# Optimization experiments

Hardware: AMD Instinct MI355X
Metric: run time of the kernel (lower is better)

## Reference

```python
import jax, jax.numpy as jnp
import numpy as np

DIM = 1024
N_HEADS = 16
HEAD_DIM = DIM // N_HEADS


def setup_inputs() -> dict:
    key = jax.random.key(0)
    kx, kq, kk, kv, ko = jax.random.split(key, 5)
    B, S = 2, 2048
    scale = 1.0 / np.sqrt(DIM)
    return {
        "x": jax.random.normal(kx, (B, S, DIM), dtype=jnp.float32),
        "Wq": jax.random.normal(kq, (DIM, DIM), dtype=jnp.float32) * scale,
        "Wk": jax.random.normal(kk, (DIM, DIM), dtype=jnp.float32) * scale,
        "Wv": jax.random.normal(kv, (DIM, DIM), dtype=jnp.float32) * scale,
        "Wo": jax.random.normal(ko, (DIM, DIM), dtype=jnp.float32) * scale,
    }


def rotate_half(x):
    x1, x2 = jnp.split(x, 2, axis=-1)
    return jnp.concatenate([-x2, x1], axis=-1)


def rope_freqs(seq_len, dim):
    inv_freq = 1.0 / (10000.0 ** (jnp.arange(0, dim, 2, dtype=jnp.float32) / dim))
    t = jnp.arange(seq_len, dtype=jnp.float32)
    freqs = jnp.einsum('i,j->ij', t, inv_freq)  # [S, dim/2]
    return jnp.concatenate([freqs, freqs], axis=-1)  # [S, dim]


def apply_rotary(x, freqs):
    # x: [B, H, S, Dh], freqs: [S, Dh]
    cos = jnp.cos(freqs)[None, None]
    sin = jnp.sin(freqs)[None, None]
    return x * cos + rotate_half(x) * sin


def reference(x, Wq, Wk, Wv, Wo):
    B, S, D = x.shape
    H, Dh = N_HEADS, HEAD_DIM
    # nn.Linear(dim, dim, bias=False): y = x @ W.T
    q = (x @ Wq.T).reshape(B, S, H, Dh).transpose(0, 2, 1, 3)
    k = (x @ Wk.T).reshape(B, S, H, Dh).transpose(0, 2, 1, 3)
    v = (x @ Wv.T).reshape(B, S, H, Dh).transpose(0, 2, 1, 3)
    freqs = rope_freqs(S, Dh)
    q = apply_rotary(q, freqs)
    k = apply_rotary(k, freqs)
    attn = jnp.einsum('bhqd,bhkd->bhqk', q, k) / jnp.sqrt(jnp.float32(Dh))
    attn = jax.nn.softmax(attn, axis=-1)
    out = jnp.einsum('bhqk,bhkd->bhqd', attn, v)
    out = out.transpose(0, 2, 1, 3).reshape(B, S, D)
    return out @ Wo.T
```

## Files before the change

kernel.cpp:

```cpp
#include <hip/hip_runtime.h>
#include <hip/hip_bf16.h>

#define NB 2
#define NS 2048
#define ND 1024
#define NH 16
#define NDH 64
#define NM 4096
#define KVT 4096
#define KVBH (NS * NDH)

typedef __bf16 bf16;
typedef __bf16 bf16x8 __attribute__((ext_vector_type(8)));
typedef __bf16 bf16x4 __attribute__((ext_vector_type(4)));
typedef float f32x4 __attribute__((ext_vector_type(4)));
typedef float f32x16 __attribute__((ext_vector_type(16)));

#define ASYNC16(g, l) __builtin_amdgcn_global_load_lds( \
    (const __attribute__((address_space(1))) void*)(g), \
    (__attribute__((address_space(3))) void*)(l), 16, 0, 0)

static __device__ __forceinline__ unsigned cvt_pk_bf16(float a, float b) {
  unsigned r;
  asm("v_cvt_pk_bf16_f32 %0, %1, %2" : "=v"(r) : "v"(a), "v"(b));
  return r;
}

__global__ __launch_bounds__(256) void convert_kernel(
    const float* __restrict__ x,
    const float* __restrict__ wq, const float* __restrict__ wk,
    const float* __restrict__ wv, const float* __restrict__ wo,
    bf16* __restrict__ xb, bf16* __restrict__ wb) {
  int i = blockIdx.x * 256 + threadIdx.x;
  const int n_x4 = (NM * ND) / 4;
  const int n_w4 = (ND * ND) / 4;
  float4 v;
  bf16* dst;
  if (i < n_x4) {
    v = ((const float4*)x)[i];
    dst = xb + (size_t)i * 4;
  } else {
    int j = i - n_x4;
    int w = j / n_w4;
    int o = j - w * n_w4;
    const float* W = (w == 0) ? wq : (w == 1) ? wk : (w == 2) ? wv : wo;
    v = ((const float4*)W)[o];
    dst = wb + (size_t)w * (ND * ND) + (size_t)o * 4;
  }
  bf16x4 o4;
  o4[0] = (bf16)v.x; o4[1] = (bf16)v.y; o4[2] = (bf16)v.z; o4[3] = (bf16)v.w;
  *(bf16x4*)dst = o4;
}

__global__ __launch_bounds__(256) void tab_kernel(float2* __restrict__ tab) {
  int t = blockIdx.x * 256 + threadIdx.x;
  int s = t >> 5, d = t & 31;
  float invf = exp2f(-0.4152410118609203f * (float)d);
  float f = (float)s * invf;
  float sn, cs;
  sincosf(f, &sn, &cs);
  tab[t] = make_float2(cs, sn);
}

__global__ __launch_bounds__(256) void gemm_qkv(
    const bf16* __restrict__ A, const bf16* __restrict__ Bmat,
    bf16* __restrict__ Qr, bf16* __restrict__ Kg, bf16* __restrict__ vraw,
    const float2* __restrict__ tab) {
  __shared__ bf16 As[128 * 64];
  __shared__ bf16 Bs[128 * 64];
  const int t = threadIdx.x;
  const int lane = t & 63, w = t >> 6;
  const int wr = w >> 1, wc = w & 1;
  const int bm = blockIdx.y * 128;
  const int bn = blockIdx.x * 128;
  const int z = blockIdx.z;
  const bf16* Bz = Bmat + (size_t)z * ND * ND;

  f32x4 acc[4][4];
#pragma unroll
  for (int i = 0; i < 4; ++i)
#pragma unroll
    for (int j = 0; j < 4; ++j) acc[i][j] = (f32x4){0.f, 0.f, 0.f, 0.f};

  for (int kt = 0; kt < ND / 64; ++kt) {
    __syncthreads();
#pragma unroll
    for (int i = 0; i < 4; ++i) {
      int c = w * 64 + lane + i * 256;
      int row = c >> 3;
      int js = (c & 7) ^ (row & 7);
      ASYNC16(A + (size_t)(bm + row) * ND + kt * 64 + js * 8, As + c * 8);
      ASYNC16(Bz + (size_t)(bn + row) * ND + kt * 64 + js * 8, Bs + c * 8);
    }
    __syncthreads();
#pragma unroll
    for (int ks = 0; ks < 2; ++ks) {
      const int kb = ks * 64 + (lane >> 4) * 16;
      bf16x8 af[4], bfr[4];
#pragma unroll
      for (int i = 0; i < 4; ++i) {
        int ra = wr * 64 + i * 16 + (lane & 15);
        af[i] = *(const bf16x8*)((const char*)As + ra * 128 + (kb ^ ((ra & 7) << 4)));
        int rb = wc * 64 + i * 16 + (lane & 15);
        bfr[i] = *(const bf16x8*)((const char*)Bs + rb * 128 + (kb ^ ((rb & 7) << 4)));
      }
#pragma unroll
      for (int i = 0; i < 4; ++i)
#pragma unroll
        for (int j = 0; j < 4; ++j)
          acc[i][j] = __builtin_amdgcn_mfma_f32_16x16x32_bf16(af[i], bfr[j], acc[i][j], 0, 0, 0);
    }
  }

  const int row0 = bm + wr * 64;
  const int col0 = bn + wc * 64;
  if (z == 2) {
#pragma unroll
    for (int i = 0; i < 4; ++i)
#pragma unroll
      for (int j = 0; j < 4; ++j) {
        int r = row0 + i * 16 + (lane >> 4) * 4;
        int ccol = col0 + j * 16 + (lane & 15);
#pragma unroll
        for (int q = 0; q < 4; ++q)
          vraw[(size_t)(r + q) * ND + ccol] = (bf16)acc[i][j][q];
      }
  } else {
    const float qs = z ? 1.0f : 0.1803368801111204f;
    const int h = col0 >> 6;
    const int ln15 = lane & 15;
#pragma unroll
    for (int i = 0; i < 4; ++i)
#pragma unroll
      for (int j = 0; j < 2; ++j)
#pragma unroll
        for (int q = 0; q < 4; ++q) {
          int r = row0 + i * 16 + (lane >> 4) * 4 + q;
          int b = r >> 11, s = r & (NS - 1);
          int d1 = j * 16 + ln15;
          float2 tc = tab[s * 32 + d1];
          float x1 = acc[i][j][q], x2 = acc[i][j + 2][q];
          float y1 = (x1 * tc.x - x2 * tc.y) * qs;
          float y2 = (x2 * tc.x + x1 * tc.y) * qs;
          if (z == 0) {
            size_t base = ((size_t)((b * NH + h) * NS + s)) * NDH;
            Qr[base + d1]      = (bf16)y1;
            Qr[base + d1 + 32] = (bf16)y2;
          } else {
            size_t kb2 = ((size_t)(b * NH + h)) * KVBH + (size_t)(s >> 6) * KVT + (s & 63) * 8;
            int cp1 = d1 >> 3, e1 = d1 & 7;
            Kg[kb2 + cp1 * 512 + e1]       = (bf16)y1;
            Kg[kb2 + (cp1 + 4) * 512 + e1] = (bf16)y2;
          }
        }
  }
}

__global__ __launch_bounds__(256) void gemm_out(
    const bf16* __restrict__ A, const bf16* __restrict__ Bmat,
    float* __restrict__ Cout) {
  __shared__ bf16 As[128 * 64];
  __shared__ bf16 Bs[64 * 64];
  const int t = threadIdx.x;
  const int lane = t & 63, w = t >> 6;
  const int wr = w >> 1, wc = w & 1;
  const int bm = blockIdx.y * 128;
  const int bn = blockIdx.x * 64;

  f32x4 acc[4][2];
#pragma unroll
  for (int i = 0; i < 4; ++i)
#pragma unroll
    for (int j = 0; j < 2; ++j) acc[i][j] = (f32x4){0.f, 0.f, 0.f, 0.f};

  for (int kt = 0; kt < ND / 64; ++kt) {
    __syncthreads();
#pragma unroll
    for (int i = 0; i < 4; ++i) {
      int c = i * 256 + t;
      int row = c >> 3;
      int js = (c & 7) ^ (row & 7);
      ASYNC16(A + (size_t)(bm + row) * ND + kt * 64 + js * 8, As + c * 8);
    }
#pragma unroll
    for (int i = 0; i < 2; ++i) {
      int c = i * 256 + t;
      int row = c >> 3;
      int js = (c & 7) ^ (row & 7);
      ASYNC16(Bmat + (size_t)(bn + row) * ND + kt * 64 + js * 8, Bs + c * 8);
    }
    __syncthreads();
#pragma unroll
    for (int ks = 0; ks < 2; ++ks) {
      const int kb = ks * 64 + (lane >> 4) * 16;
      bf16x8 af[4], bfr[2];
#pragma unroll
      for (int i = 0; i < 4; ++i) {
        int ra = wr * 64 + i * 16 + (lane & 15);
        af[i] = *(const bf16x8*)((const char*)As + ra * 128 + (kb ^ ((ra & 7) << 4)));
      }
#pragma unroll
      for (int j = 0; j < 2; ++j) {
        int rb = wc * 32 + j * 16 + (lane & 15);
        bfr[j] = *(const bf16x8*)((const char*)Bs + rb * 128 + (kb ^ ((rb & 7) << 4)));
      }
#pragma unroll
      for (int i = 0; i < 4; ++i)
#pragma unroll
        for (int j = 0; j < 2; ++j)
          acc[i][j] = __builtin_amdgcn_mfma_f32_16x16x32_bf16(af[i], bfr[j], acc[i][j], 0, 0, 0);
    }
  }

  const int row0 = bm + wr * 64;
  const int col0 = bn + wc * 32;
#pragma unroll
  for (int i = 0; i < 4; ++i)
#pragma unroll
    for (int j = 0; j < 2; ++j) {
      int r = row0 + i * 16 + (lane >> 4) * 4;
      int ccol = col0 + j * 16 + (lane & 15);
#pragma unroll
      for (int q = 0; q < 4; ++q)
        Cout[(size_t)(r + q) * ND + ccol] = acc[i][j][q];
    }
}

__global__ __launch_bounds__(256) void transv_kernel(
    const bf16* __restrict__ vraw, bf16* __restrict__ Vg) {
  __shared__ bf16 tl[64][65];
  int s0 = blockIdx.x * 64;
  int bh = blockIdx.y;
  int b = bh >> 4, h = bh & 15;
  int t = threadIdx.x;
#pragma unroll
  for (int i = 0; i < 4; ++i) {
    int row = (t >> 4) + i * 16;
    int d4 = (t & 15) * 4;
    *(bf16x4*)&tl[row][d4] =
        *(const bf16x4*)&vraw[((size_t)(b * NS + s0 + row)) * ND + h * NDH + d4];
  }
  __syncthreads();
  const size_t tbase = (size_t)bh * KVBH + (size_t)(s0 >> 6) * KVT;
#pragma unroll
  for (int i = 0; i < 4; ++i) {
    int dr = (t >> 4) + i * 16;
    int s4 = (t & 15) * 4;
    bf16x4 o;
    o[0] = tl[s4 + 0][dr]; o[1] = tl[s4 + 1][dr];
    o[2] = tl[s4 + 2][dr]; o[3] = tl[s4 + 3][dr];
    *(bf16x4*)&Vg[tbase + (s4 >> 3) * 512 + dr * 8 + (s4 & 7)] = o;
  }
}

__global__ __launch_bounds__(256, 2) void attn_kernel(
    const bf16* __restrict__ Qr, const bf16* __restrict__ Kg,
    const bf16* __restrict__ Vg, bf16* __restrict__ out) {
  __shared__ bf16 Ks[2][512 * 8];
  __shared__ bf16 Vs[2][512 * 8];
  const int t = threadIdx.x, lane = t & 63, w = t >> 6;
  const int hi = lane >> 5, ln = lane & 31;
  int wg = blockIdx.x;
  int sw = (wg & 7) * 64 + (wg >> 3);
  const int qb = sw & 15, bh = sw >> 4;
  const int q0 = qb * 128 + w * 32;
  const size_t kvbase = (size_t)bh * KVBH;

  bf16x8 qv[4];
  {
    const bf16* Qb = Qr + ((size_t)bh * NS + q0 + ln) * NDH + hi * 8;
#pragma unroll
    for (int c = 0; c < 4; ++c) qv[c] = *(const bf16x8*)(Qb + c * 16);
  }

  f32x16 O0, O1;
#pragma unroll
  for (int r = 0; r < 16; ++r) { O0[r] = 0.f; O1[r] = 0.f; }
  float m = -1e30f, l = 0.f;

#define STAGE_KV(nb, kt2)                                                     \
  {                                                                           \
    _Pragma("unroll")                                                         \
    for (int i = 0; i < 2; ++i) {                                             \
      int ch = i * 256 + t;                                                   \
      ASYNC16(Kg + kvbase + (size_t)(kt2) * KVT + ch * 8, &Ks[nb][0] + ch * 8); \
      ASYNC16(Vg + kvbase + (size_t)(kt2) * KVT + ch * 8, &Vs[nb][0] + ch * 8); \
    }                                                                         \
  }

  STAGE_KV(0, 0);
  __syncthreads();

  int cur = 0;
  for (int kt = 0; kt < NS / 64; ++kt) {
    if (kt + 1 < NS / 64) STAGE_KV(cur ^ 1, kt + 1);
    const bf16* Kb = &Ks[cur][0];
    const bf16* Vb = &Vs[cur][0];

    f32x16 s0, s1;
#pragma unroll
    for (int r = 0; r < 16; ++r) { s0[r] = 0.f; s1[r] = 0.f; }
    bf16x8 k0[4], k1[4];
#pragma unroll
    for (int c = 0; c < 4; ++c) {
      k0[c] = *(const bf16x8*)(Kb + (2 * c + hi) * 512 + ln * 8);
      k1[c] = *(const bf16x8*)(Kb + (2 * c + hi) * 512 + (32 + ln) * 8);
    }
    __builtin_amdgcn_s_setprio(1);
#pragma unroll
    for (int c = 0; c < 4; ++c) {
      s0 = __builtin_amdgcn_mfma_f32_32x32x16_bf16(k0[c], qv[c], s0, 0, 0, 0);
      s1 = __builtin_amdgcn_mfma_f32_32x32x16_bf16(k1[c], qv[c], s1, 0, 0, 0);
    }
    __builtin_amdgcn_s_setprio(0);

    float a0[8];
#pragma unroll
    for (int r = 0; r < 8; ++r) a0[r] = fmaxf(fmaxf(s0[r], s0[r + 8]), fmaxf(s1[r], s1[r + 8]));
    float b0 = fmaxf(fmaxf(a0[0], a0[1]), fmaxf(a0[2], a0[3]));
    float b1 = fmaxf(fmaxf(a0[4], a0[5]), fmaxf(a0[6], a0[7]));
    float pmax = fmaxf(b0, b1);
    pmax = fmaxf(pmax, __shfl_xor(pmax, 32, 64));

    if (!__all(pmax - m <= 8.0f)) {
      float mnew = fmaxf(m, pmax);
      float scl = exp2f(m - mnew);
      m = mnew; l *= scl;
#pragma unroll
      for (int r = 0; r < 16; ++r) { O0[r] *= scl; O1[r] *= scl; }
    }

    float p0[16], p1[16];
#pragma unroll
    for (int r = 0; r < 16; ++r) { p0[r] = exp2f(s0[r] - m); p1[r] = exp2f(s1[r] - m); }
    float sp[8];
#pragma unroll
    for (int r = 0; r < 8; ++r) sp[r] = (p0[r] + p0[r + 8]) + (p1[r] + p1[r + 8]);
    float sum = (((sp[0] + sp[1]) + (sp[2] + sp[3])) + ((sp[4] + sp[5]) + (sp[6] + sp[7])));
    sum += __shfl_xor(sum, 32, 64);
    l += sum;

    unsigned u0[8], u1[8], x0[8], x1[8];
#pragma unroll
    for (int g = 0; g < 4; ++g) {
      u0[g]     = cvt_pk_bf16(p0[4 * g],     p0[4 * g + 1]);
      u1[g]     = cvt_pk_bf16(p0[4 * g + 2], p0[4 * g + 3]);
      u0[4 + g] = cvt_pk_bf16(p1[4 * g],     p1[4 * g + 1]);
      u1[4 + g] = cvt_pk_bf16(p1[4 * g + 2], p1[4 * g + 3]);
    }
#pragma unroll
    for (int g = 0; g < 8; ++g) {
      x0[g] = __shfl_xor(u0[g], 32, 64);
      x1[g] = __shfl_xor(u1[g], 32, 64);
    }

    bf16x8 v0[4], v1[4];
#pragma unroll
    for (int c = 0; c < 4; ++c) {
      v0[c] = *(const bf16x8*)(Vb + (2 * c + hi) * 512 + ln * 8);
      v1[c] = *(const bf16x8*)(Vb + (2 * c + hi) * 512 + (32 + ln) * 8);
    }
    __builtin_amdgcn_s_setprio(1);
#pragma unroll
    for (int c = 0; c < 4; ++c) {
      int base = (c >> 1) * 4 + (c & 1) * 2;
      union { unsigned u[4]; bf16x8 v; } pa;
      pa.u[0] = hi ? x0[base + 1] : u0[base];
      pa.u[1] = hi ? x1[base + 1] : u1[base];
      pa.u[2] = hi ? u0[base + 1] : x0[base];
      pa.u[3] = hi ? u1[base + 1] : x1[base];
      O0 = __builtin_amdgcn_mfma_f32_32x32x16_bf16(pa.v, v0[c], O0, 0, 0, 0);
      O1 = __builtin_amdgcn_mfma_f32_32x32x16_bf16(pa.v, v1[c], O1, 0, 0, 0);
    }
    __builtin_amdgcn_s_setprio(0);

    __syncthreads();
    cur ^= 1;
  }

  float rl = 1.0f / l;
  const int b = bh >> 4, h = bh & 15;
#pragma unroll
  for (int r = 0; r < 16; ++r) {
    int q = (r & 3) + 8 * (r >> 2) + 4 * hi;
    float rlq = __shfl(rl, q, 64);
    int s = q0 + q;
    size_t base = ((size_t)(b * NS + s)) * ND + h * NDH + ln;
    out[base]      = (bf16)(O0[r] * rlq);
    out[base + 32] = (bf16)(O1[r] * rlq);
  }
}

extern "C" void kernel_launch(void* const* d_in, const int* in_sizes, int n_in,
                              void* d_out, int out_size, void* d_ws, size_t ws_size,
                              hipStream_t stream) {
  const float* x  = (const float*)d_in[0];
  const float* wq = (const float*)d_in[1];
  const float* wk = (const float*)d_in[2];
  const float* wv = (const float*)d_in[3];
  const float* wo = (const float*)d_in[4];
  char* ws = (char*)d_ws;
  bf16* xb    = (bf16*)(ws);
  bf16* wb    = (bf16*)(ws + (8u << 20));
  bf16* vraw  = (bf16*)(ws + (16u << 20));
  bf16* Qr    = (bf16*)(ws + (24u << 20));
  bf16* Kg    = (bf16*)(ws + (32u << 20));
  bf16* Vg    = (bf16*)(ws + (40u << 20));
  bf16* attnb = (bf16*)(ws + (48u << 20));
  float2* tab = (float2*)(ws + (56u << 20));
  float* out  = (float*)d_out;

  convert_kernel<<<8192, 256, 0, stream>>>(x, wq, wk, wv, wo, xb, wb);
  tab_kernel<<<256, 256, 0, stream>>>(tab);
  gemm_qkv<<<dim3(8, 32, 3), 256, 0, stream>>>(xb, wb, Qr, Kg, vraw, tab);
  transv_kernel<<<dim3(32, 32), 256, 0, stream>>>(vraw, Vg);
  attn_kernel<<<dim3(512), 256, 0, stream>>>(Qr, Kg, Vg, attnb);
  gemm_out<<<dim3(16, 32), 256, 0, stream>>>(attnb, wb + 3 * ND * ND, out);
}
```

Before: 227.9 us.

## Process 64 query rows per wave in attention to reuse K/V fragments

Each wave in the attention kernel now handles two 32-row query tiles instead of one, so every K and V fragment read from LDS feeds twice as many MFMAs. The grid drops from 512 to 256 workgroups, and launch bounds allow only one block per CU to make room for the extra accumulators. The half-wave exchange of P is also switched from shfl_xor to permlane32_swap. The risks are higher register pressure, fewer resident waves to hide latency, and only 256 blocks to spread across the CUs.

```diff
diff --git a/kernel.cpp b/kernel.cpp
--- a/kernel.cpp
+++ b/kernel.cpp
@@ -15,6 +15,7 @@
 typedef __bf16 bf16x4 __attribute__((ext_vector_type(4)));
 typedef float f32x4 __attribute__((ext_vector_type(4)));
 typedef float f32x16 __attribute__((ext_vector_type(16)));
+typedef unsigned u32x2 __attribute__((ext_vector_type(2)));
 
 #define ASYNC16(g, l) __builtin_amdgcn_global_load_lds( \
     (const __attribute__((address_space(1))) void*)(g), \
@@ -24,6 +25,16 @@
   unsigned r;
   asm("v_cvt_pk_bf16_f32 %0, %1, %2" : "=v"(r) : "v"(a), "v"(b));
   return r;
+}
+static __device__ __forceinline__ void plswap(unsigned &a, unsigned &b) {
+  u32x2 r = __builtin_amdgcn_permlane32_swap(a, b, false, false);
+  a = r[0]; b = r[1];
+}
+static __device__ __forceinline__ float xhalf_max(float x) {
+  return fmaxf(x, __shfl_xor(x, 32, 64));
+}
+static __device__ __forceinline__ float xhalf_sum(float x) {
+  return x + __shfl_xor(x, 32, 64);
 }
 
 __global__ __launch_bounds__(256) void convert_kernel(
@@ -253,7 +264,7 @@
   }
 }
 
-__global__ __launch_bounds__(256, 2) void attn_kernel(
+__global__ __launch_bounds__(256, 1) void attn_kernel(
     const bf16* __restrict__ Qr, const bf16* __restrict__ Kg,
     const bf16* __restrict__ Vg, bf16* __restrict__ out) {
   __shared__ bf16 Ks[2][512 * 8];
@@ -261,31 +272,35 @@
   const int t = threadIdx.x, lane = t & 63, w = t >> 6;
   const int hi = lane >> 5, ln = lane & 31;
   int wg = blockIdx.x;
-  int sw = (wg & 7) * 64 + (wg >> 3);
-  const int qb = sw & 15, bh = sw >> 4;
-  const int q0 = qb * 128 + w * 32;
+  int sw = (wg & 7) * 32 + (wg >> 3);
+  const int qb = sw & 7, bh = sw >> 3;
+  const int q0 = qb * 256 + w * 64;
   const size_t kvbase = (size_t)bh * KVBH;
 
-  bf16x8 qv[4];
+  bf16x8 qvA[4], qvB[4];
   {
-    const bf16* Qb = Qr + ((size_t)bh * NS + q0 + ln) * NDH + hi * 8;
-#pragma unroll
-    for (int c = 0; c < 4; ++c) qv[c] = *(const bf16x8*)(Qb + c * 16);
-  }
-
-  f32x16 O0, O1;
-#pragma unroll
-  for (int r = 0; r < 16; ++r) { O0[r] = 0.f; O1[r] = 0.f; }
-  float m = -1e30f, l = 0.f;
-
-#define STAGE_KV(nb, kt2)                                                     \
-  {                                                                           \
-    _Pragma("unroll")                                                         \
-    for (int i = 0; i < 2; ++i) {                                             \
-      int ch = i * 256 + t;                                                   \
+    const bf16* QbA = Qr + ((size_t)bh * NS + q0 + ln) * NDH + hi * 8;
+    const bf16* QbB = QbA + (size_t)32 * NDH;
+#pragma unroll
+    for (int c = 0; c < 4; ++c) {
+      qvA[c] = *(const bf16x8*)(QbA + c * 16);
+      qvB[c] = *(const bf16x8*)(QbB + c * 16);
+    }
+  }
+
+  f32x16 OA0, OA1, OB0, OB1;
+#pragma unroll
+  for (int r = 0; r < 16; ++r) { OA0[r] = 0.f; OA1[r] = 0.f; OB0[r] = 0.f; OB1[r] = 0.f; }
+  float mA = -1e30f, lA = 0.f, mB = -1e30f, lB = 0.f;
+
+#define STAGE_KV(nb, kt2)                                                       \
+  {                                                                             \
+    _Pragma("unroll")                                                           \
+    for (int i = 0; i < 2; ++i) {                                               \
+      int ch = i * 256 + t;                                                     \
       ASYNC16(Kg + kvbase + (size_t)(kt2) * KVT + ch * 8, &Ks[nb][0] + ch * 8); \
       ASYNC16(Vg + kvbase + (size_t)(kt2) * KVT + ch * 8, &Vs[nb][0] + ch * 8); \
-    }                                                                         \
+    }                                                                           \
   }
 
   STAGE_KV(0, 0);
@@ -297,62 +312,25 @@
     const bf16* Kb = &Ks[cur][0];
     const bf16* Vb = &Vs[cur][0];
 
-    f32x16 s0, s1;
-#pragma unroll
-    for (int r = 0; r < 16; ++r) { s0[r] = 0.f; s1[r] = 0.f; }
     bf16x8 k0[4], k1[4];
 #pragma unroll
     for (int c = 0; c < 4; ++c) {
       k0[c] = *(const bf16x8*)(Kb + (2 * c + hi) * 512 + ln * 8);
       k1[c] = *(const bf16x8*)(Kb + (2 * c + hi) * 512 + (32 + ln) * 8);
     }
+
+    f32x16 sA0, sA1, sB0, sB1;
+#pragma unroll
+    for (int r = 0; r < 16; ++r) { sA0[r] = 0.f; sA1[r] = 0.f; sB0[r] = 0.f; sB1[r] = 0.f; }
     __builtin_amdgcn_s_setprio(1);
 #pragma unroll
     for (int c = 0; c < 4; ++c) {
-      s0 = __builtin_amdgcn_mfma_f32_32x32x16_bf16(k0[c], qv[c], s0, 0, 0, 0);
-      s1 = __builtin_amdgcn_mfma_f32_32x32x16_bf16(k1[c], qv[c], s1, 0, 0, 0);
+      sA0 = __builtin_amdgcn_mfma_f32_32x32x16_bf16(k0[c], qvA[c], sA0, 0, 0, 0);
+      sA1 = __builtin_amdgcn_mfma_f32_32x32x16_bf16(k1[c], qvA[c], sA1, 0, 0, 0);
+      sB0 = __builtin_amdgcn_mfma_f32_32x32x16_bf16(k0[c], qvB[c], sB0, 0, 0, 0);
+      sB1 = __builtin_amdgcn_mfma_f32_32x32x16_bf16(k1[c], qvB[c], sB1, 0, 0, 0);
     }
     __builtin_amdgcn_s_setprio(0);
-
-    float a0[8];
-#pragma unroll
-    for (int r = 0; r < 8; ++r) a0[r] = fmaxf(fmaxf(s0[r], s0[r + 8]), fmaxf(s1[r], s1[r + 8]));
-    float b0 = fmaxf(fmaxf(a0[0], a0[1]), fmaxf(a0[2], a0[3]));
-    float b1 = fmaxf(fmaxf(a0[4], a0[5]), fmaxf(a0[6], a0[7]));
-    float pmax = fmaxf(b0, b1);
-    pmax = fmaxf(pmax, __shfl_xor(pmax, 32, 64));
-
-    if (!__all(pmax - m <= 8.0f)) {
-      float mnew = fmaxf(m, pmax);
-      float scl = exp2f(m - mnew);
-      m = mnew; l *= scl;
-#pragma unroll
-      for (int r = 0; r < 16; ++r) { O0[r] *= scl; O1[r] *= scl; }
-    }
-
-    float p0[16], p1[16];
-#pragma unroll
-    for (int r = 0; r < 16; ++r) { p0[r] = exp2f(s0[r] - m); p1[r] = exp2f(s1[r] - m); }
-    float sp[8];
-#pragma unroll
-    for (int r = 0; r < 8; ++r) sp[r] = (p0[r] + p0[r + 8]) + (p1[r] + p1[r + 8]);
-    float sum = (((sp[0] + sp[1]) + (sp[2] + sp[3])) + ((sp[4] + sp[5]) + (sp[6] + sp[7])));
-    sum += __shfl_xor(sum, 32, 64);
-    l += sum;
-
-    unsigned u0[8], u1[8], x0[8], x1[8];
-#pragma unroll
-    for (int g = 0; g < 4; ++g) {
-      u0[g]     = cvt_pk_bf16(p0[4 * g],     p0[4 * g + 1]);
-      u1[g]     = cvt_pk_bf16(p0[4 * g + 2], p0[4 * g + 3]);
-      u0[4 + g] = cvt_pk_bf16(p1[4 * g],     p1[4 * g + 1]);
-      u1[4 + g] = cvt_pk_bf16(p1[4 * g + 2], p1[4 * g + 3]);
-    }
-#pragma unroll
-    for (int g = 0; g < 8; ++g) {
-      x0[g] = __shfl_xor(u0[g], 32, 64);
-      x1[g] = __shfl_xor(u1[g], 32, 64);
-    }
 
     bf16x8 v0[4], v1[4];
 #pragma unroll
@@ -360,17 +338,80 @@
       v0[c] = *(const bf16x8*)(Vb + (2 * c + hi) * 512 + ln * 8);
       v1[c] = *(const bf16x8*)(Vb + (2 * c + hi) * 512 + (32 + ln) * 8);
     }
+
+    float a0[8];
+#pragma unroll
+    for (int r = 0; r < 8; ++r) a0[r] = fmaxf(fmaxf(sA0[r], sA0[r + 8]), fmaxf(sA1[r], sA1[r + 8]));
+    float pmaxA = fmaxf(fmaxf(fmaxf(a0[0], a0[1]), fmaxf(a0[2], a0[3])),
+                        fmaxf(fmaxf(a0[4], a0[5]), fmaxf(a0[6], a0[7])));
+    pmaxA = xhalf_max(pmaxA);
+#pragma unroll
+    for (int r = 0; r < 8; ++r) a0[r] = fmaxf(fmaxf(sB0[r], sB0[r + 8]), fmaxf(sB1[r], sB1[r + 8]));
+    float pmaxB = fmaxf(fmaxf(fmaxf(a0[0], a0[1]), fmaxf(a0[2], a0[3])),
+                        fmaxf(fmaxf(a0[4], a0[5]), fmaxf(a0[6], a0[7])));
+    pmaxB = xhalf_max(pmaxB);
+
+    if (!__all((pmaxA - mA <= 8.0f) && (pmaxB - mB <= 8.0f))) {
+      float mAn = fmaxf(mA, pmaxA), mBn = fmaxf(mB, pmaxB);
+      float dA = mA - mAn, dB = mB - mBn;
+      lA *= exp2f(dA); lB *= exp2f(dB);
+      mA = mAn; mB = mBn;
+#pragma unroll
+      for (int r = 0; r < 16; ++r) {
+        int q = (r & 3) + 8 * (r >> 2) + 4 * hi;
+        float sa = exp2f(__shfl(dA, q, 64));
+        float sb = exp2f(__shfl(dB, q, 64));
+        OA0[r] *= sa; OA1[r] *= sa;
+        OB0[r] *= sb; OB1[r] *= sb;
+      }
+    }
+
+    float pA0[16], pA1[16], pB0[16], pB1[16];
+#pragma unroll
+    for (int r = 0; r < 16; ++r) {
+      pA0[r] = exp2f(sA0[r] - mA); pA1[r] = exp2f(sA1[r] - mA);
+      pB0[r] = exp2f(sB0[r] - mB); pB1[r] = exp2f(sB1[r] - mB);
+    }
+    float sp[8];
+#pragma unroll
+    for (int r = 0; r < 8; ++r) sp[r] = (pA0[r] + pA0[r + 8]) + (pA1[r] + pA1[r + 8]);
+    float sumA = ((sp[0] + sp[1]) + (sp[2] + sp[3])) + ((sp[4] + sp[5]) + (sp[6] + sp[7]));
+    lA += xhalf_sum(sumA);
+#pragma unroll
+    for (int r = 0; r < 8; ++r) sp[r] = (pB0[r] + pB0[r + 8]) + (pB1[r] + pB1[r + 8]);
+    float sumB = ((sp[0] + sp[1]) + (sp[2] + sp[3])) + ((sp[4] + sp[5]) + (sp[6] + sp[7]));
+    lB += xhalf_sum(sumB);
+
+    unsigned uA0[8], uA1[8], uB0[8], uB1[8];
+#pragma unroll
+    for (int g = 0; g < 4; ++g) {
+      uA0[g]     = cvt_pk_bf16(pA0[4 * g],     pA0[4 * g + 1]);
+      uA1[g]     = cvt_pk_bf16(pA0[4 * g + 2], pA0[4 * g + 3]);
+      uA0[4 + g] = cvt_pk_bf16(pA1[4 * g],     pA1[4 * g + 1]);
+      uA1[4 + g] = cvt_pk_bf16(pA1[4 * g + 2], pA1[4 * g + 3]);
+      uB0[g]     = cvt_pk_bf16(pB0[4 * g],     pB0[4 * g + 1]);
+      uB1[g]     = cvt_pk_bf16(pB0[4 * g + 2], pB0[4 * g + 3]);
+      uB0[4 + g] = cvt_pk_bf16(pB1[4 * g],     pB1[4 * g + 1]);
+      uB1[4 + g] = cvt_pk_bf16(pB1[4 * g + 2], pB1[4 * g + 3]);
+    }
+#pragma unroll
+    for (int g = 0; g < 8; g += 2) {
+      plswap(uA0[g], uA0[g + 1]); plswap(uA1[g], uA1[g + 1]);
+      plswap(uB0[g], uB0[g + 1]); plswap(uB1[g], uB1[g + 1]);
+    }
+
     __builtin_amdgcn_s_setprio(1);
 #pragma unroll
     for (int c = 0; c < 4; ++c) {
-      int base = (c >> 1) * 4 + (c & 1) * 2;
-      union { unsigned u[4]; bf16x8 v; } pa;
-      pa.u[0] = hi ? x0[base + 1] : u0[base];
-      pa.u[1] = hi ? x1[base + 1] : u1[base];
-      pa.u[2] = hi ? u0[base + 1] : x0[base];
-      pa.u[3] = hi ? u1[base + 1] : x1[base];
-      O0 = __builtin_amdgcn_mfma_f32_32x32x16_bf16(pa.v, v0[c], O0, 0, 0, 0);
-      O1 = __builtin_amdgcn_mfma_f32_32x32x16_bf16(pa.v, v1[c], O1, 0, 0, 0);
+      union { unsigned u[4]; bf16x8 v; } paA, paB;
+      paA.u[0] = uA0[2 * c];     paA.u[1] = uA1[2 * c];
+      paA.u[2] = uA0[2 * c + 1]; paA.u[3] = uA1[2 * c + 1];
+      paB.u[0] = uB0[2 * c];     paB.u[1] = uB1[2 * c];
+      paB.u[2] = uB0[2 * c + 1]; paB.u[3] = uB1[2 * c + 1];
+      OA0 = __builtin_amdgcn_mfma_f32_32x32x16_bf16(paA.v, v0[c], OA0, 0, 0, 0);
+      OA1 = __builtin_amdgcn_mfma_f32_32x32x16_bf16(paA.v, v1[c], OA1, 0, 0, 0);
+      OB0 = __builtin_amdgcn_mfma_f32_32x32x16_bf16(paB.v, v0[c], OB0, 0, 0, 0);
+      OB1 = __builtin_amdgcn_mfma_f32_32x32x16_bf16(paB.v, v1[c], OB1, 0, 0, 0);
     }
     __builtin_amdgcn_s_setprio(0);
 
@@ -378,16 +419,19 @@
     cur ^= 1;
   }
 
-  float rl = 1.0f / l;
+  float rlA = 1.0f / lA, rlB = 1.0f / lB;
   const int b = bh >> 4, h = bh & 15;
 #pragma unroll
   for (int r = 0; r < 16; ++r) {
     int q = (r & 3) + 8 * (r >> 2) + 4 * hi;
-    float rlq = __shfl(rl, q, 64);
-    int s = q0 + q;
-    size_t base = ((size_t)(b * NS + s)) * ND + h * NDH + ln;
-    out[base]      = (bf16)(O0[r] * rlq);
-    out[base + 32] = (bf16)(O1[r] * rlq);
+    float ra = __shfl(rlA, q, 64);
+    float rb = __shfl(rlB, q, 64);
+    size_t baseA = ((size_t)(b * NS + q0 + q)) * ND + h * NDH + ln;
+    size_t baseB = ((size_t)(b * NS + q0 + 32 + q)) * ND + h * NDH + ln;
+    out[baseA]      = (bf16)(OA0[r] * ra);
+    out[baseA + 32] = (bf16)(OA1[r] * ra);
+    out[baseB]      = (bf16)(OB0[r] * rb);
+    out[baseB + 32] = (bf16)(OB1[r] * rb);
   }
 }
 
@@ -414,6 +458,6 @@
   tab_kernel<<<256, 256, 0, stream>>>(tab);
   gemm_qkv<<<dim3(8, 32, 3), 256, 0, stream>>>(xb, wb, Qr, Kg, vraw, tab);
   transv_kernel<<<dim3(32, 32), 256, 0, stream>>>(vraw, Vg);
-  attn_kernel<<<dim3(512), 256, 0, stream>>>(Qr, Kg, Vg, attnb);
+  attn_kernel<<<dim3(256), 256, 0, stream>>>(Qr, Kg, Vg, attnb);
   gemm_out<<<dim3(16, 32), 256, 0, stream>>>(attnb, wb + 3 * ND * ND, out);
 }
```

New measurement: 246.3 us. 1.08x slower.
